# Performance work log

Measured on AMD Instinct MI355X. Metric: run time of the kernel, lower is better.

The kernel has to match this reference:

```python
import jax, jax.numpy as jnp
import numpy as np

D = 8        # q_ndim (= dof_ndim)
HID = 200    # hidden_size
N = 16384    # batch of states
EPS = 0.1    # qdot regularizer coefficient in L()


def _lagrangian(z, Ws, bs):
    # z: (2D,) = [q, qdot]; angular_dims=() so CosSin is an identity pass-through
    v = z[D:]
    h = z
    for W, b in zip(Ws[:-1], bs[:-1]):
        h = jax.nn.softplus(h @ W + b)   # FCsoftplus blocks
    L = (h @ Ws[-1] + bs[-1])[0]          # final Linear -> scalar (Reshape(-1))
    return L + EPS * jnp.dot(v, v)


def setup_inputs():
    key = jax.random.key(0)
    ks = jax.random.split(key, 5)
    z = jax.random.normal(ks[0], (N, 2 * D), dtype=jnp.float32)
    t = jnp.zeros((), dtype=jnp.float32)

    def lin(k, fi, fo, scale):
        return (jax.random.normal(k, (fi, fo), dtype=jnp.float32)
                * jnp.float32(scale / np.sqrt(fi)))

    W0 = lin(ks[1], 2 * D, HID, 1.0)
    W1 = lin(ks[2], HID, HID, 1.0)
    W2 = lin(ks[3], HID, HID, 1.0)
    W3 = lin(ks[4], HID, 1, 0.01)  # small head keeps mass matrix M well conditioned
    b0 = jnp.zeros((HID,), jnp.float32)  # zero_bias init per FCsoftplus/Linear
    b1 = jnp.zeros((HID,), jnp.float32)
    b2 = jnp.zeros((HID,), jnp.float32)
    b3 = jnp.zeros((1,), jnp.float32)
    return dict(t=t, z=z, W0=W0, b0=b0, W1=W1, b1=b1, W2=W2, b2=b2, W3=W3, b3=b3)


def reference(t, z, W0, b0, W1, b1, W2, b2, W3, b3):
    # Euler-Lagrange dynamics (LagrangianDynamics):
    #   M a = dL/dq - (d2L/dq dv) v,  M = d2L/dv2;  dz/dt = [v, a]
    Ws = (W0, W1, W2, W3)
    bs = (b0, b1, b2, b3)
    Lfn = lambda zz: _lagrangian(zz, Ws, bs)

    def dyn_single(zi):
        g = jax.grad(Lfn)(zi)              # (2D,)  = [dL/dq, dL/dv]
        H = jax.jacfwd(jax.grad(Lfn))(zi)  # (2D,2D) Hessian of L wrt z
        v = zi[D:]
        M = H[D:, D:]                      # d(dL/dv)/dv  -> mass matrix
        C = H[D:, :D]                      # d(dL/dv)/dq
        F = g[:D] - C @ v
        a = jnp.linalg.solve(M, F)
        return jnp.concatenate([v, a])     # (2D,)

    return jax.vmap(dyn_single)(z)         # (N, 2D)
```

## Files before the change

### kernel.cpp

```cpp
#include <hip/hip_runtime.h>
#include <math.h>

#define DD 8
#define ZD 16
#define HID 200
#define EPSL 0.1f
#define BS 16
#define NTHREADS 1024
#define NKC 7
#define NMT 13
#define XSTR 216
#define CSTR 212
#define HSTR 20
#define WSTR 208
#define NTAN 8
#define NT4 4

#define KSC 1024.0f
#define SSC 64.0f
#define INV_K (1.0f/1024.0f)
#define INV_KS (1.0f/65536.0f)

typedef _Float16 half8 __attribute__((ext_vector_type(8)));
typedef _Float16 half4v __attribute__((ext_vector_type(4)));
typedef _Float16 half2v __attribute__((ext_vector_type(2)));
typedef float float4v __attribute__((ext_vector_type(4)));

#define S4 (NKC*NMT*64*8)
#define OFF_W1T 0
#define OFF_W2T (S4)
#define OFF_W1  (2*S4)
#define OFF_W2  (3*S4)
#define OFF_W0T (4*S4)
#define OFF_W0  (4*S4 + NMT*64*8)
#define WS_HALFS (4*S4 + NMT*64*8 + NKC*64*8)

__global__ void prep(const float* __restrict__ W0, const float* __restrict__ W1,
                     const float* __restrict__ W2, _Float16* __restrict__ ws)
{
    int idx = blockIdx.x * 256 + threadIdx.x;
    if (idx >= WS_HALFS) return;
    float v = 0.f;
    if (idx < 4*S4) {
        int arr = idx / S4, e = idx % S4;
        int kc = e / (NMT*64*8); int r = e % (NMT*64*8);
        int mt = r / (64*8); r %= 64*8;
        int lane = r / 8, j = r % 8;
        int m = mt*16 + (lane & 15);
        int k = kc*32 + (lane >> 4)*8 + j;
        if (m < HID && k < HID) {
            if      (arr == 0) v = W1[k*HID + m];
            else if (arr == 1) v = W2[k*HID + m];
            else if (arr == 2) v = W1[m*HID + k];
            else               v = W2[m*HID + k];
        }
    } else if (idx < OFF_W0) {
        int e = idx - OFF_W0T;
        int mt = e / (64*8); int r = e % (64*8);
        int lane = r / 8, j = r % 8;
        int m = mt*16 + (lane & 15);
        int k = (lane >> 4)*8 + j;
        if (m < HID && k < ZD) v = W0[k*HID + m];
    } else {
        int e = idx - OFF_W0;
        int kc = e / (64*8); int r = e % (64*8);
        int lane = r / 8, j = r % 8;
        int m = (lane & 15);
        int k = kc*32 + (lane >> 4)*8 + j;
        if (k < HID) v = W0[m*HID + k];
    }
    ws[idx] = (_Float16)v;
}

__device__ __forceinline__ half4v pk4(float4v a) {
    half2v lo = __builtin_bit_cast(half2v, __builtin_amdgcn_cvt_pkrtz(a.x, a.y));
    half2v hi = __builtin_bit_cast(half2v, __builtin_amdgcn_cvt_pkrtz(a.z, a.w));
    return __builtin_shufflevector(lo, hi, 0, 1, 2, 3);
}
__device__ __forceinline__ void sig_sp(float x, float& sp, float& sg) {
    float e = __expf(-fabsf(x));
    float r = 1.0f / (1.0f + e);
    sg = (x >= 0.f) ? r : (1.0f - r);
    sp = fmaxf(x, 0.f) + __logf(1.f + e);
}

template<int NTILES, int MTC>
__device__ __forceinline__ void run_mv(const half8* __restrict__ Asw,
                                       const _Float16* __restrict__ Xsrc,
                                       int mt0, int lane,
                                       float4v acc[2][NTILES])
{
    const int lm = lane & 15, q = lane >> 4;
    constexpr int PF = (NTILES > 1) ? 3 : NKC;
#pragma unroll
    for (int m = 0; m < MTC; ++m)
#pragma unroll
        for (int n = 0; n < NTILES; ++n)
            acc[m][n] = (float4v){0.f, 0.f, 0.f, 0.f};

    half8 a[MTC][PF];
#pragma unroll
    for (int p = 0; p < PF; ++p)
#pragma unroll
        for (int m = 0; m < MTC; ++m)
            a[m][p] = Asw[(p*NMT + mt0 + m)*64 + lane];

    half8 x[NTILES];
#pragma unroll
    for (int n = 0; n < NTILES; ++n)
        x[n] = *(const half8*)(Xsrc + (n*16 + lm)*XSTR + q*8);

#pragma unroll
    for (int kc = 0; kc < NKC; ++kc) {
        half8 xn[NTILES];
        if (kc + 1 < NKC)
#pragma unroll
            for (int n = 0; n < NTILES; ++n)
                xn[n] = *(const half8*)(Xsrc + (n*16 + lm)*XSTR + (kc+1)*32 + q*8);
        half8 an[MTC];
        if (kc + PF < NKC)
#pragma unroll
            for (int m = 0; m < MTC; ++m)
                an[m] = Asw[((kc+PF)*NMT + mt0 + m)*64 + lane];

#pragma unroll
        for (int m = 0; m < MTC; ++m)
#pragma unroll
            for (int n = 0; n < NTILES; ++n)
                acc[m][n] = __builtin_amdgcn_mfma_f32_16x16x32_f16(a[m][0], x[n], acc[m][n], 0, 0, 0);

        if (kc + 1 < NKC) {
#pragma unroll
            for (int m = 0; m < MTC; ++m)
#pragma unroll
                for (int p = 0; p + 1 < PF; ++p) a[m][p] = a[m][p+1];
            if (kc + PF < NKC)
#pragma unroll
                for (int m = 0; m < MTC; ++m) a[m][PF-1] = an[m];
#pragma unroll
            for (int n = 0; n < NTILES; ++n) x[n] = xn[n];
        }
    }
}

__global__ void __launch_bounds__(NTHREADS, 4)
lnn_main(const float* __restrict__ z,
         const float* __restrict__ W0, const float* __restrict__ b0,
         const float* __restrict__ b1, const float* __restrict__ b2,
         const float* __restrict__ W3,
         const _Float16* __restrict__ ws,
         float* __restrict__ out)
{
    __shared__ alignas(16) _Float16 Xt[128*XSTR];
    __shared__ alignas(16) _Float16 Xb[128*XSTR];
    __shared__ alignas(16) _Float16 Cf[5][16*CSTR];
    __shared__ alignas(16) _Float16 Xz[16*40];
    __shared__ alignas(16) _Float16 bsh[4*WSTR];
    __shared__ alignas(16) _Float16 w0t[NTAN*WSTR];
    __shared__ alignas(16) float gsh[16*HSTR];
    __shared__ alignas(16) float Hr[128*HSTR];

    const int tid  = threadIdx.x;
    const int wave = tid >> 6;
    const int lane = tid & 63;
    const int lm   = lane & 15;
    const int q    = lane >> 4;
    const int s0   = blockIdx.x * BS;

    const int twm  = wave >> 1;
    const int twn  = wave & 1;
    const int mt0t = (twm < 5) ? twm*2 : (twm + 5);
    const int mtct = (twm < 5) ? 2 : 1;

    const half8* W1Tsw = (const half8*)(ws + OFF_W1T);
    const half8* W2Tsw = (const half8*)(ws + OFF_W2T);
    const half8* W1sw  = (const half8*)(ws + OFF_W1);
    const half8* W2sw  = (const half8*)(ws + OFF_W2);
    const half8* W0Tsw = (const half8*)(ws + OFF_W0T);
    const half8* W0sw  = (const half8*)(ws + OFF_W0);

    if (tid < 256) {
        int s = tid >> 4, k = tid & 15;
        Xz[s*40 + k]      = (_Float16)z[(s0 + s)*ZD + k];
        Xz[s*40 + 16 + k] = (_Float16)0.f;
    }
    for (int idx = tid; idx < 128*16; idx += NTHREADS) {
        int r = idx >> 4, c = 200 + (idx & 15);
        Xt[r*XSTR + c] = (_Float16)0.f;
        Xb[r*XSTR + c] = (_Float16)0.f;
    }
    if (tid < 8) {
        Xt[16*XSTR + tid] = (_Float16)0.f;
        Xb[16*XSTR + tid] = (_Float16)0.f;
    }
    for (int idx = tid; idx < 4*WSTR; idx += NTHREADS) {
        int l = idx / WSTR, u = idx % WSTR;
        float v = 0.f;
        if (u < HID) {
            if      (l == 0) v = b0[u];
            else if (l == 1) v = b1[u];
            else if (l == 2) v = b2[u];
            else             v = KSC * W3[u];
        }
        bsh[idx] = (_Float16)v;
    }
    for (int idx = tid; idx < NTAN*WSTR; idx += NTHREADS) {
        int t = idx / WSTR, u = idx % WSTR;
        w0t[idx] = (_Float16)((u < HID) ? SSC * W0[(DD + t)*HID + u] : 0.f);
    }
    __syncthreads();

    float4v acc1[2][1];
    const int ubf = wave*16 + q*4;

    if (wave < NMT) {
        acc1[0][0] = (float4v){0.f,0.f,0.f,0.f};
        half8 xz = *(const half8*)(Xz + lm*40 + q*8);
        half8 a = W0Tsw[wave*64 + lane];
        acc1[0][0] = __builtin_amdgcn_mfma_f32_16x16x32_f16(a, xz, acc1[0][0], 0, 0, 0);
        half4v bb = *(const half4v*)(&bsh[0*WSTR + ubf]);
        float h[4], p[4];
#pragma unroll
        for (int r = 0; r < 4; ++r) {
            float av = acc1[0][0][r] + (float)bb[r];
            sig_sp(av, h[r], p[r]);
        }
        *(half4v*)(&Xt[lm*XSTR + ubf])     = pk4((float4v){h[0],h[1],h[2],h[3]});
        *(half4v*)(&Cf[0][lm*CSTR + ubf])  = pk4((float4v){p[0],p[1],p[2],p[3]});
    }
    __syncthreads();

    if (wave < NMT) run_mv<1,1>(W1Tsw, Xt, wave, lane, acc1);
    __syncthreads();
    if (wave < NMT) {
        half4v bb = *(const half4v*)(&bsh[1*WSTR + ubf]);
        float h[4], p[4];
#pragma unroll
        for (int r = 0; r < 4; ++r) {
            float av = acc1[0][0][r] + (float)bb[r];
            sig_sp(av, h[r], p[r]);
        }
        *(half4v*)(&Xt[lm*XSTR + ubf])    = pk4((float4v){h[0],h[1],h[2],h[3]});
        *(half4v*)(&Cf[1][lm*CSTR + ubf]) = pk4((float4v){p[0],p[1],p[2],p[3]});
    }
    __syncthreads();

    if (wave < NMT) run_mv<1,1>(W2Tsw, Xt, wave, lane, acc1);
    __syncthreads();
    if (wave < NMT) {
        half4v bb = *(const half4v*)(&bsh[2*WSTR + ubf]);
        half4v w3 = *(const half4v*)(&bsh[3*WSTR + ubf]);
        float d2[4], c2[4];
#pragma unroll
        for (int r = 0; r < 4; ++r) {
            float av = acc1[0][0][r] + (float)bb[r];
            float e = __expf(-fabsf(av));
            float rr = 1.f / (1.f + e);
            float sg = (av >= 0.f) ? rr : (1.f - rr);
            float wk = (float)w3[r];
            d2[r] = wk * sg;
            c2[r] = wk * sg * (1.f - sg);
        }
        *(half4v*)(&Xt[lm*XSTR + ubf])    = pk4((float4v){d2[0],d2[1],d2[2],d2[3]});
        *(half4v*)(&Cf[2][lm*CSTR + ubf]) = pk4((float4v){c2[0],c2[1],c2[2],c2[3]});
    }
    __syncthreads();

    if (wave < NMT) run_mv<1,1>(W2sw, Xt, wave, lane, acc1);
    __syncthreads();
    if (wave < NMT) {
        half4v p1 = *(const half4v*)(&Cf[1][lm*CSTR + ubf]);
        half4v u1 = pk4(acc1[0][0]);
        half4v one = {(_Float16)1.f,(_Float16)1.f,(_Float16)1.f,(_Float16)1.f};
        *(half4v*)(&Xt[lm*XSTR + ubf])    = u1 * p1;
        *(half4v*)(&Cf[3][lm*CSTR + ubf]) = u1 * (one - p1);
    }
    __syncthreads();

    if (wave < NMT) run_mv<1,1>(W1sw, Xt, wave, lane, acc1);
    __syncthreads();
    if (wave < NMT) {
        half4v p0 = *(const half4v*)(&Cf[0][lm*CSTR + ubf]);
        half4v u0 = pk4(acc1[0][0]);
        half4v one = {(_Float16)1.f,(_Float16)1.f,(_Float16)1.f,(_Float16)1.f};
        half4v d0 = u0 * p0;
        *(half4v*)(&Xt[lm*XSTR + ubf])    = d0;
        *(half4v*)(&Cf[4][lm*CSTR + ubf]) = d0 * (one - p0);
    }
    __syncthreads();

    if (wave == 0) {
        half8 aw[NKC];
#pragma unroll
        for (int kc = 0; kc < NKC; ++kc) aw[kc] = W0sw[kc*64 + lane];
        float4v g = (float4v){0.f,0.f,0.f,0.f};
#pragma unroll
        for (int kc = 0; kc < NKC; ++kc) {
            half8 x = *(const half8*)(Xt + lm*XSTR + kc*32 + q*8);
            g = __builtin_amdgcn_mfma_f32_16x16x32_f16(aw[kc], x, g, 0, 0, 0);
        }
        float4v gv; gv.x = g.x*INV_K; gv.y = g.y*INV_K; gv.z = g.z*INV_K; gv.w = g.w*INV_K;
        *(float4v*)(&gsh[lm*HSTR + q*4]) = gv;
    } else {
        for (int idx = tid - 64; idx < 128*50; idx += NTHREADS - 64) {
            int row = idx / 50, u = (idx % 50)*4;
            int s = row & 15, t = row >> 4;
            half4v p0 = *(const half4v*)(&Cf[0][s*CSTR + u]);
            half4v w0 = *(const half4v*)(&w0t[t*WSTR + u]);
            *(half4v*)(&Xb[row*XSTR + u]) = p0 * w0;
        }
    }
    __syncthreads();

    float4v acc4[2][NT4];

    if (mtct == 2) run_mv<NT4,2>(W1Tsw, Xb + twn*64*XSTR, mt0t, lane, acc4);
    else           run_mv<NT4,1>(W1Tsw, Xb + twn*64*XSTR, mt0t, lane, acc4);
#pragma unroll
    for (int m = 0; m < 2; ++m)
        if (m < mtct) {
            const int ub = (mt0t + m)*16 + q*4;
            half4v p1 = *(const half4v*)(&Cf[1][lm*CSTR + ub]);
#pragma unroll
            for (int n = 0; n < NT4; ++n) {
                int row = (twn*NT4 + n)*16 + lm;
                *(half4v*)(&Xt[row*XSTR + ub]) = pk4(acc4[m][n]) * p1;
            }
        }
    __syncthreads();

    if (mtct == 2) run_mv<NT4,2>(W2Tsw, Xt + twn*64*XSTR, mt0t, lane, acc4);
    else           run_mv<NT4,1>(W2Tsw, Xt + twn*64*XSTR, mt0t, lane, acc4);
#pragma unroll
    for (int m = 0; m < 2; ++m)
        if (m < mtct) {
            const int ub = (mt0t + m)*16 + q*4;
            half4v c2 = *(const half4v*)(&Cf[2][lm*CSTR + ub]);
#pragma unroll
            for (int n = 0; n < NT4; ++n) {
                int row = (twn*NT4 + n)*16 + lm;
                *(half4v*)(&Xb[row*XSTR + ub]) = pk4(acc4[m][n]) * c2;
            }
        }
    __syncthreads();

    if (mtct == 2) run_mv<NT4,2>(W2sw, Xb + twn*64*XSTR, mt0t, lane, acc4);
    else           run_mv<NT4,1>(W2sw, Xb + twn*64*XSTR, mt0t, lane, acc4);
    __syncthreads();
#pragma unroll
    for (int m = 0; m < 2; ++m)
        if (m < mtct) {
            const int ub = (mt0t + m)*16 + q*4;
            half4v p1 = *(const half4v*)(&Cf[1][lm*CSTR + ub]);
            half4v c3 = *(const half4v*)(&Cf[3][lm*CSTR + ub]);
#pragma unroll
            for (int n = 0; n < NT4; ++n) {
                int row = (twn*NT4 + n)*16 + lm;
                half4v th1 = *(const half4v*)(&Xt[row*XSTR + ub]);
                *(half4v*)(&Xb[row*XSTR + ub]) = pk4(acc4[m][n]) * p1 + c3 * th1;
            }
        }
    __syncthreads();

    if (mtct == 2) run_mv<NT4,2>(W1sw, Xb + twn*64*XSTR, mt0t, lane, acc4);
    else           run_mv<NT4,1>(W1sw, Xb + twn*64*XSTR, mt0t, lane, acc4);
#pragma unroll
    for (int m = 0; m < 2; ++m)
        if (m < mtct) {
            const int ub = (mt0t + m)*16 + q*4;
            half4v p0 = *(const half4v*)(&Cf[0][lm*CSTR + ub]);
            half4v c4 = *(const half4v*)(&Cf[4][lm*CSTR + ub]);
#pragma unroll
            for (int n = 0; n < NT4; ++n) {
                int row = (twn*NT4 + n)*16 + lm;
                half4v w0 = *(const half4v*)(&w0t[(twn*NT4 + n)*WSTR + ub]);
                *(half4v*)(&Xt[row*XSTR + ub]) = pk4(acc4[m][n]) * p0 + c4 * w0;
            }
        }
    __syncthreads();

    if (wave < 8) {
        half8 aw[NKC];
#pragma unroll
        for (int kc = 0; kc < NKC; ++kc) aw[kc] = W0sw[kc*64 + lane];
        float4v hacc = (float4v){0.f,0.f,0.f,0.f};
#pragma unroll
        for (int kc = 0; kc < NKC; ++kc) {
            half8 x = *(const half8*)(Xt + (wave*16 + lm)*XSTR + kc*32 + q*8);
            hacc = __builtin_amdgcn_mfma_f32_16x16x32_f16(aw[kc], x, hacc, 0, 0, 0);
        }
        int row = wave*16 + lm;
        float4v hv;
        hv.x = hacc.x*INV_KS; hv.y = hacc.y*INV_KS;
        hv.z = hacc.z*INV_KS; hv.w = hacc.w*INV_KS;
        *(float4v*)(&Hr[row*HSTR + q*4]) = hv;
    }
    __syncthreads();

    if (tid < BS) {
        const int s = tid;
        float M[DD][DD], F[DD], v[DD], a[DD];
#pragma unroll
        for (int c = 0; c < DD; ++c) v[c] = z[(s0 + s)*ZD + DD + c];
#pragma unroll
        for (int r = 0; r < DD; ++r) {
            float f = gsh[s*HSTR + r];
#pragma unroll
            for (int c = 0; c < DD; ++c) {
                M[r][c] = Hr[(r*16 + s)*HSTR + DD + c] + ((r == c) ? 2.f*EPSL : 0.f);
                f -= Hr[(r*16 + s)*HSTR + c] * v[c];
            }
            F[r] = f;
        }
#pragma unroll
        for (int col = 0; col < DD; ++col) {
            const float inv = 1.f / M[col][col];
#pragma unroll
            for (int r = col + 1; r < DD; ++r) {
                const float fac = M[r][col] * inv;
#pragma unroll
                for (int c = col + 1; c < DD; ++c) M[r][c] -= fac * M[col][c];
                F[r] -= fac * F[col];
            }
        }
#pragma unroll
        for (int r = DD - 1; r >= 0; --r) {
            float ssum = F[r];
#pragma unroll
            for (int c = r + 1; c < DD; ++c) ssum -= M[r][c] * a[c];
            a[r] = ssum / M[r][r];
        }
        float* op = out + (size_t)(s0 + s)*ZD;
#pragma unroll
        for (int c = 0; c < DD; ++c) { op[c] = v[c]; op[DD + c] = a[c]; }
    }
}

extern "C" void kernel_launch(void* const* d_in, const int* in_sizes, int n_in,
                              void* d_out, int out_size, void* d_ws, size_t ws_size,
                              hipStream_t stream)
{
    const float* z  = (const float*)d_in[1];
    const float* W0 = (const float*)d_in[2];
    const float* b0 = (const float*)d_in[3];
    const float* W1 = (const float*)d_in[4];
    const float* b1 = (const float*)d_in[5];
    const float* W2 = (const float*)d_in[6];
    const float* b2 = (const float*)d_in[7];
    const float* W3 = (const float*)d_in[8];
    float* out = (float*)d_out;
    _Float16* ws = (_Float16*)d_ws;

    const int n = in_sizes[1] / (2*DD);

    prep<<<dim3((WS_HALFS + 255)/256), dim3(256), 0, stream>>>(W0, W1, W2, ws);
    lnn_main<<<dim3(n / BS), dim3(NTHREADS), 0, stream>>>(
        z, W0, b0, b1, b2, W3, ws, out);
}
```

Baseline: 160.1 us.

## Remap tangent matvecs to one M-tile per wave and ping-pong LDS buffers

The tangent (Hessian) pass now gives each of the 13 waves one weight M-tile across all 8 tangent column tiles, replacing the old 2D split over 16 waves with uneven M-tiles. The forward/backward single-column passes now alternate between the Xt and Xb buffers, which removes the extra barrier between each matvec and its epilogue. The c3*th1 product is kept in registers rather than being reread from LDS. Three waves now sit idle during the tangent GEMMs, and more accumulator and register state is live per wave, which can hurt occupancy.

Result: slower. 172.4 us (+7.7%).

```diff
diff --git a/kernel.cpp b/kernel.cpp
--- a/kernel.cpp
+++ b/kernel.cpp
@@ -14,7 +14,7 @@
 #define HSTR 20
 #define WSTR 208
 #define NTAN 8
-#define NT4 4
+#define NT8 8
 
 #define KSC 1024.0f
 #define SSC 64.0f
@@ -88,10 +88,10 @@
 __device__ __forceinline__ void run_mv(const half8* __restrict__ Asw,
                                        const _Float16* __restrict__ Xsrc,
                                        int mt0, int lane,
-                                       float4v acc[2][NTILES])
+                                       float4v acc[MTC][NTILES])
 {
     const int lm = lane & 15, q = lane >> 4;
-    constexpr int PF = (NTILES > 1) ? 3 : NKC;
+    constexpr int PF = (NTILES > 1) ? 2 : NKC;
 #pragma unroll
     for (int m = 0; m < MTC; ++m)
 #pragma unroll
@@ -105,41 +105,29 @@
         for (int m = 0; m < MTC; ++m)
             a[m][p] = Asw[(p*NMT + mt0 + m)*64 + lane];
 
-    half8 x[NTILES];
-#pragma unroll
-    for (int n = 0; n < NTILES; ++n)
-        x[n] = *(const half8*)(Xsrc + (n*16 + lm)*XSTR + q*8);
-
 #pragma unroll
     for (int kc = 0; kc < NKC; ++kc) {
-        half8 xn[NTILES];
-        if (kc + 1 < NKC)
-#pragma unroll
-            for (int n = 0; n < NTILES; ++n)
-                xn[n] = *(const half8*)(Xsrc + (n*16 + lm)*XSTR + (kc+1)*32 + q*8);
+        half8 x[NTILES];
+#pragma unroll
+        for (int n = 0; n < NTILES; ++n)
+            x[n] = *(const half8*)(Xsrc + (n*16 + lm)*XSTR + kc*32 + q*8);
         half8 an[MTC];
         if (kc + PF < NKC)
 #pragma unroll
             for (int m = 0; m < MTC; ++m)
                 an[m] = Asw[((kc+PF)*NMT + mt0 + m)*64 + lane];
-
 #pragma unroll
         for (int m = 0; m < MTC; ++m)
 #pragma unroll
             for (int n = 0; n < NTILES; ++n)
                 acc[m][n] = __builtin_amdgcn_mfma_f32_16x16x32_f16(a[m][0], x[n], acc[m][n], 0, 0, 0);
-
-        if (kc + 1 < NKC) {
-#pragma unroll
-            for (int m = 0; m < MTC; ++m)
-#pragma unroll
-                for (int p = 0; p + 1 < PF; ++p) a[m][p] = a[m][p+1];
-            if (kc + PF < NKC)
-#pragma unroll
-                for (int m = 0; m < MTC; ++m) a[m][PF-1] = an[m];
-#pragma unroll
-            for (int n = 0; n < NTILES; ++n) x[n] = xn[n];
-        }
+#pragma unroll
+        for (int m = 0; m < MTC; ++m)
+#pragma unroll
+            for (int p = 0; p + 1 < PF; ++p) a[m][p] = a[m][p+1];
+        if (kc + PF < NKC)
+#pragma unroll
+            for (int m = 0; m < MTC; ++m) a[m][PF-1] = an[m];
     }
 }
 
@@ -167,11 +155,6 @@
     const int q    = lane >> 4;
     const int s0   = blockIdx.x * BS;
 
-    const int twm  = wave >> 1;
-    const int twn  = wave & 1;
-    const int mt0t = (twm < 5) ? twm*2 : (twm + 5);
-    const int mtct = (twm < 5) ? 2 : 1;
-
     const half8* W1Tsw = (const half8*)(ws + OFF_W1T);
     const half8* W2Tsw = (const half8*)(ws + OFF_W2T);
     const half8* W1sw  = (const half8*)(ws + OFF_W1);
@@ -210,7 +193,7 @@
     }
     __syncthreads();
 
-    float4v acc1[2][1];
+    float4v acc1[1][1];
     const int ubf = wave*16 + q*4;
 
     if (wave < NMT) {
@@ -230,9 +213,8 @@
     }
     __syncthreads();
 
-    if (wave < NMT) run_mv<1,1>(W1Tsw, Xt, wave, lane, acc1);
-    __syncthreads();
-    if (wave < NMT) {
+    if (wave < NMT) {
+        run_mv<1,1>(W1Tsw, Xt, wave, lane, acc1);
         half4v bb = *(const half4v*)(&bsh[1*WSTR + ubf]);
         float h[4], p[4];
 #pragma unroll
@@ -240,14 +222,13 @@
             float av = acc1[0][0][r] + (float)bb[r];
             sig_sp(av, h[r], p[r]);
         }
-        *(half4v*)(&Xt[lm*XSTR + ubf])    = pk4((float4v){h[0],h[1],h[2],h[3]});
+        *(half4v*)(&Xb[lm*XSTR + ubf])    = pk4((float4v){h[0],h[1],h[2],h[3]});
         *(half4v*)(&Cf[1][lm*CSTR + ubf]) = pk4((float4v){p[0],p[1],p[2],p[3]});
     }
     __syncthreads();
 
-    if (wave < NMT) run_mv<1,1>(W2Tsw, Xt, wave, lane, acc1);
-    __syncthreads();
-    if (wave < NMT) {
+    if (wave < NMT) {
+        run_mv<1,1>(W2Tsw, Xb, wave, lane, acc1);
         half4v bb = *(const half4v*)(&bsh[2*WSTR + ubf]);
         half4v w3 = *(const half4v*)(&bsh[3*WSTR + ubf]);
         float d2[4], c2[4];
@@ -266,20 +247,18 @@
     }
     __syncthreads();
 
-    if (wave < NMT) run_mv<1,1>(W2sw, Xt, wave, lane, acc1);
-    __syncthreads();
-    if (wave < NMT) {
+    if (wave < NMT) {
+        run_mv<1,1>(W2sw, Xt, wave, lane, acc1);
         half4v p1 = *(const half4v*)(&Cf[1][lm*CSTR + ubf]);
         half4v u1 = pk4(acc1[0][0]);
         half4v one = {(_Float16)1.f,(_Float16)1.f,(_Float16)1.f,(_Float16)1.f};
-        *(half4v*)(&Xt[lm*XSTR + ubf])    = u1 * p1;
+        *(half4v*)(&Xb[lm*XSTR + ubf])    = u1 * p1;
         *(half4v*)(&Cf[3][lm*CSTR + ubf]) = u1 * (one - p1);
     }
     __syncthreads();
 
-    if (wave < NMT) run_mv<1,1>(W1sw, Xt, wave, lane, acc1);
-    __syncthreads();
-    if (wave < NMT) {
+    if (wave < NMT) {
+        run_mv<1,1>(W1sw, Xb, wave, lane, acc1);
         half4v p0 = *(const half4v*)(&Cf[0][lm*CSTR + ubf]);
         half4v u0 = pk4(acc1[0][0]);
         half4v one = {(_Float16)1.f,(_Float16)1.f,(_Float16)1.f,(_Float16)1.f};
@@ -312,71 +291,50 @@
     }
     __syncthreads();
 
-    float4v acc4[2][NT4];
-
-    if (mtct == 2) run_mv<NT4,2>(W1Tsw, Xb + twn*64*XSTR, mt0t, lane, acc4);
-    else           run_mv<NT4,1>(W1Tsw, Xb + twn*64*XSTR, mt0t, lane, acc4);
-#pragma unroll
-    for (int m = 0; m < 2; ++m)
-        if (m < mtct) {
-            const int ub = (mt0t + m)*16 + q*4;
-            half4v p1 = *(const half4v*)(&Cf[1][lm*CSTR + ub]);
-#pragma unroll
-            for (int n = 0; n < NT4; ++n) {
-                int row = (twn*NT4 + n)*16 + lm;
-                *(half4v*)(&Xt[row*XSTR + ub]) = pk4(acc4[m][n]) * p1;
-            }
-        }
-    __syncthreads();
-
-    if (mtct == 2) run_mv<NT4,2>(W2Tsw, Xt + twn*64*XSTR, mt0t, lane, acc4);
-    else           run_mv<NT4,1>(W2Tsw, Xt + twn*64*XSTR, mt0t, lane, acc4);
-#pragma unroll
-    for (int m = 0; m < 2; ++m)
-        if (m < mtct) {
-            const int ub = (mt0t + m)*16 + q*4;
-            half4v c2 = *(const half4v*)(&Cf[2][lm*CSTR + ub]);
-#pragma unroll
-            for (int n = 0; n < NT4; ++n) {
-                int row = (twn*NT4 + n)*16 + lm;
-                *(half4v*)(&Xb[row*XSTR + ub]) = pk4(acc4[m][n]) * c2;
-            }
-        }
-    __syncthreads();
-
-    if (mtct == 2) run_mv<NT4,2>(W2sw, Xb + twn*64*XSTR, mt0t, lane, acc4);
-    else           run_mv<NT4,1>(W2sw, Xb + twn*64*XSTR, mt0t, lane, acc4);
-    __syncthreads();
-#pragma unroll
-    for (int m = 0; m < 2; ++m)
-        if (m < mtct) {
-            const int ub = (mt0t + m)*16 + q*4;
-            half4v p1 = *(const half4v*)(&Cf[1][lm*CSTR + ub]);
-            half4v c3 = *(const half4v*)(&Cf[3][lm*CSTR + ub]);
-#pragma unroll
-            for (int n = 0; n < NT4; ++n) {
-                int row = (twn*NT4 + n)*16 + lm;
-                half4v th1 = *(const half4v*)(&Xt[row*XSTR + ub]);
-                *(half4v*)(&Xb[row*XSTR + ub]) = pk4(acc4[m][n]) * p1 + c3 * th1;
-            }
-        }
-    __syncthreads();
-
-    if (mtct == 2) run_mv<NT4,2>(W1sw, Xb + twn*64*XSTR, mt0t, lane, acc4);
-    else           run_mv<NT4,1>(W1sw, Xb + twn*64*XSTR, mt0t, lane, acc4);
-#pragma unroll
-    for (int m = 0; m < 2; ++m)
-        if (m < mtct) {
-            const int ub = (mt0t + m)*16 + q*4;
-            half4v p0 = *(const half4v*)(&Cf[0][lm*CSTR + ub]);
-            half4v c4 = *(const half4v*)(&Cf[4][lm*CSTR + ub]);
-#pragma unroll
-            for (int n = 0; n < NT4; ++n) {
-                int row = (twn*NT4 + n)*16 + lm;
-                half4v w0 = *(const half4v*)(&w0t[(twn*NT4 + n)*WSTR + ub]);
-                *(half4v*)(&Xt[row*XSTR + ub]) = pk4(acc4[m][n]) * p0 + c4 * w0;
-            }
-        }
+    float4v acc8[1][NT8];
+    half4v c3th1[NT8];
+
+    if (wave < NMT) {
+        run_mv<NT8,1>(W1Tsw, Xb, wave, lane, acc8);
+        half4v p1 = *(const half4v*)(&Cf[1][lm*CSTR + ubf]);
+        half4v c3 = *(const half4v*)(&Cf[3][lm*CSTR + ubf]);
+#pragma unroll
+        for (int n = 0; n < NT8; ++n) {
+            half4v t = pk4(acc8[0][n]) * p1;
+            *(half4v*)(&Xt[(n*16 + lm)*XSTR + ubf]) = t;
+            c3th1[n] = c3 * t;
+        }
+    }
+    __syncthreads();
+
+    if (wave < NMT) {
+        run_mv<NT8,1>(W2Tsw, Xt, wave, lane, acc8);
+        half4v c2 = *(const half4v*)(&Cf[2][lm*CSTR + ubf]);
+#pragma unroll
+        for (int n = 0; n < NT8; ++n)
+            *(half4v*)(&Xb[(n*16 + lm)*XSTR + ubf]) = pk4(acc8[0][n]) * c2;
+    }
+    __syncthreads();
+
+    if (wave < NMT) {
+        run_mv<NT8,1>(W2sw, Xb, wave, lane, acc8);
+        half4v p1 = *(const half4v*)(&Cf[1][lm*CSTR + ubf]);
+#pragma unroll
+        for (int n = 0; n < NT8; ++n)
+            *(half4v*)(&Xt[(n*16 + lm)*XSTR + ubf]) = pk4(acc8[0][n]) * p1 + c3th1[n];
+    }
+    __syncthreads();
+
+    if (wave < NMT) {
+        run_mv<NT8,1>(W1sw, Xt, wave, lane, acc8);
+        half4v p0 = *(const half4v*)(&Cf[0][lm*CSTR + ubf]);
+        half4v c4 = *(const half4v*)(&Cf[4][lm*CSTR + ubf]);
+#pragma unroll
+        for (int n = 0; n < NT8; ++n) {
+            half4v w0 = *(const half4v*)(&w0t[n*WSTR + ubf]);
+            *(half4v*)(&Xb[(n*16 + lm)*XSTR + ubf]) = pk4(acc8[0][n]) * p0 + c4 * w0;
+        }
+    }
     __syncthreads();
 
     if (wave < 8) {
@@ -386,7 +344,7 @@
         float4v hacc = (float4v){0.f,0.f,0.f,0.f};
 #pragma unroll
         for (int kc = 0; kc < NKC; ++kc) {
-            half8 x = *(const half8*)(Xt + (wave*16 + lm)*XSTR + kc*32 + q*8);
+            half8 x = *(const half8*)(Xb + (wave*16 + lm)*XSTR + kc*32 + q*8);
             hacc = __builtin_amdgcn_mfma_f32_16x16x32_f16(aw[kc], x, hacc, 0, 0, 0);
         }
         int row = wave*16 + lm;
```
